# Optimization experiments

Measured on AMD Instinct MI355X. Metric: run time of the kernel, lower is better.

Reference implementation:

```python
import jax, jax.numpy as jnp
import numpy as np

B, L, DIM = 2, 2048, 1024
H, D = 16, 64  # n_heads, head_dim; H*D == DIM


def setup_inputs() -> dict:
    key = jax.random.key(0)
    ks = jax.random.split(key, 5)
    s = 0.02
    return {
        "x": jax.random.normal(ks[0], (B, L, DIM), dtype=jnp.float32),
        "Wq": jax.random.normal(ks[1], (DIM, H * D), dtype=jnp.float32) * s,
        "Wk": jax.random.normal(ks[2], (DIM, H * D), dtype=jnp.float32) * s,
        "Wv": jax.random.normal(ks[3], (DIM, H * D), dtype=jnp.float32) * s,
        "Wo": jax.random.normal(ks[4], (H * D, DIM), dtype=jnp.float32) * s,
    }


def reference(x, Wq, Wk, Wv, Wo):
    b, l, _ = x.shape
    scale = 1.0 / np.sqrt(D).astype(np.float32)
    # QKV projections -> [b, h, l, d]
    q = (x @ Wq).reshape(b, l, H, D).transpose(0, 2, 1, 3)
    k = (x @ Wk).reshape(b, l, H, D).transpose(0, 2, 1, 3)
    v = (x @ Wv).reshape(b, l, H, D).transpose(0, 2, 1, 3)
    # dense scores [b, h, l, l]
    scores = jnp.einsum("bhqd,bhkd->bhqk", q, k)
    # diagonal mask: each token cannot attend to itself
    diag = jnp.eye(l, dtype=bool)  # [l, l]
    scores = jnp.where(diag, -jnp.inf, scores)
    attn = jax.nn.softmax(scores * scale, axis=-1)
    out = jnp.einsum("bhqk,bhkd->bhqd", attn, v)
    out = out.transpose(0, 2, 1, 3).reshape(b, l, H * D)
    return out @ Wo
```

## Files before the change

### kernel.cpp

```cpp
#include <hip/hip_runtime.h>
#include <hip/hip_bf16.h>
#include <math.h>

#define L_SEQ 2048
#define DIMN  1024
#define NH    16
#define HD    64
#define NB    2
#define NTOK  (NB * L_SEQ)

typedef __attribute__((ext_vector_type(8))) short bf16x8;
typedef __attribute__((ext_vector_type(4))) float f32x4;
typedef __attribute__((ext_vector_type(16))) float f32x16;
typedef __attribute__((ext_vector_type(4))) short short4v;
typedef __attribute__((ext_vector_type(2))) unsigned uint32x2;

__device__ __forceinline__ short f2bf(float x) {
  return (short)__bfloat16_as_ushort(__float2bfloat16(x));
}

__device__ __forceinline__ unsigned cvt_pk_bf16(float lo, float hi) {
  unsigned r;
  asm("v_cvt_pk_bf16_f32 %0, %1, %2" : "=v"(r) : "v"(lo), "v"(hi));
  return r;
}

__device__ __forceinline__ void permlane32_swap(unsigned& a, unsigned& b) {
  asm volatile("v_permlane32_swap_b32 %0, %1" : "+v"(a), "+v"(b));
}

__device__ __forceinline__ void gload_lds16(const short* gsrc, char* lds_dst) {
  __builtin_amdgcn_global_load_lds(
      (const __attribute__((address_space(1))) void*)gsrc,
      (__attribute__((address_space(3))) void*)lds_dst, 16, 0, 0);
}

__global__ __launch_bounds__(256) void cast_x_k(const float* __restrict__ in,
                                                short* __restrict__ out) {
  const int i = (blockIdx.x * 256 + threadIdx.x) * 8;
  float4 a = *(const float4*)(in + i);
  float4 b = *(const float4*)(in + i + 4);
  bf16x8 o;
  o[0] = f2bf(a.x); o[1] = f2bf(a.y); o[2] = f2bf(a.z); o[3] = f2bf(a.w);
  o[4] = f2bf(b.x); o[5] = f2bf(b.y); o[6] = f2bf(b.z); o[7] = f2bf(b.w);
  *(bf16x8*)(out + i) = o;
}

__global__ __launch_bounds__(256) void castT_k(const float* __restrict__ W,
                                               short* __restrict__ Wt) {
  __shared__ float s[64][65];
  const int tid = threadIdx.x;
  const int k0 = blockIdx.y * 64, n0 = blockIdx.x * 64;
#pragma unroll
  for (int i = 0; i < 4; ++i) {
    int idx = i * 256 + tid;
    int r = idx >> 4, c = (idx & 15) * 4;
    float4 v = *(const float4*)(W + (size_t)(k0 + r) * DIMN + n0 + c);
    s[r][c] = v.x; s[r][c + 1] = v.y; s[r][c + 2] = v.z; s[r][c + 3] = v.w;
  }
  __syncthreads();
#pragma unroll
  for (int i = 0; i < 4; ++i) {
    int idx = i * 256 + tid;
    int r = idx >> 4, c = (idx & 15) * 4;
    short4v o = { f2bf(s[c][r]), f2bf(s[c + 1][r]), f2bf(s[c + 2][r]), f2bf(s[c + 3][r]) };
    *(short4v*)(Wt + (size_t)(n0 + r) * DIMN + k0 + c) = o;
  }
}

__global__ __launch_bounds__(256) void vT_k(const short* __restrict__ V,
                                            short* __restrict__ Vt) {
  __shared__ short s[64][72];
  const int tid = threadIdx.x;
  const int bh = blockIdx.y;
  const int l0 = blockIdx.x * 64;
  const int row = tid >> 2, c0 = (tid & 3) * 16;
  const short* Vh = V + (size_t)bh * L_SEQ * HD;
  bf16x8 a = *(const bf16x8*)(Vh + (size_t)(l0 + row) * HD + c0);
  bf16x8 b = *(const bf16x8*)(Vh + (size_t)(l0 + row) * HD + c0 + 8);
#pragma unroll
  for (int j = 0; j < 8; ++j) { s[c0 + j][row] = a[j]; s[c0 + 8 + j][row] = b[j]; }
  __syncthreads();
  short* Vth = Vt + (size_t)bh * HD * L_SEQ;
  bf16x8 o0 = *(const bf16x8*)&s[row][c0];
  bf16x8 o1 = *(const bf16x8*)&s[row][c0 + 8];
  *(bf16x8*)(Vth + (size_t)row * L_SEQ + l0 + c0) = o0;
  *(bf16x8*)(Vth + (size_t)row * L_SEQ + l0 + c0 + 8) = o1;
}

template <int MODE>
__global__ __launch_bounds__(256) void mm_k(const short* __restrict__ A,
                                            const short* __restrict__ B0,
                                            const short* __restrict__ B1,
                                            const short* __restrict__ B2,
                                            void* __restrict__ C0,
                                            void* __restrict__ C1,
                                            void* __restrict__ C2,
                                            float scale0) {
  __shared__ char smem[65536];
  const int tid  = threadIdx.x;
  const int lane = tid & 63, wv = tid >> 6;
  const int g = lane >> 4, r16 = lane & 15;
  const int wr = wv >> 1, wc = wv & 1;
  const int row0 = blockIdx.y * 128, col0 = blockIdx.x * 128;
  const int z = blockIdx.z;
  const short* Bt = (z == 0) ? B0 : (z == 1 ? B1 : B2);
  const float scale = (MODE == 0 && z == 0) ? scale0 : 1.0f;

  f32x4 acc[4][4];
#pragma unroll
  for (int mi = 0; mi < 4; ++mi)
#pragma unroll
    for (int ni = 0; ni < 4; ++ni) acc[mi][ni] = (f32x4){0.f, 0.f, 0.f, 0.f};

  auto stage = [&](int buf, int kt) {
    const int k0 = kt * 64;
    char* As = smem + buf * 32768;
    char* Bs = As + 16384;
#pragma unroll
    for (int j = 0; j < 4; ++j) {
      const int o = j * 4096 + wv * 1024 + lane * 16;
      const int row = o >> 7;
      const int slot = (o >> 4) & 7;
      const int ksrc = k0 + ((slot ^ (row & 7)) << 3);
      gload_lds16(A  + (size_t)(row0 + row) * DIMN + ksrc, As + j * 4096 + wv * 1024);
      gload_lds16(Bt + (size_t)(col0 + row) * DIMN + ksrc, Bs + j * 4096 + wv * 1024);
    }
  };

  auto compute = [&](int buf) {
    const char* As = smem + buf * 32768;
    const char* Bs = As + 16384;
#pragma unroll
    for (int ks = 0; ks < 2; ++ks) {
      bf16x8 a[4], b[4];
#pragma unroll
      for (int mi = 0; mi < 4; ++mi) {
        const int row = wr * 64 + mi * 16 + r16;
        const int slot = (ks * 4 + g) ^ (row & 7);
        a[mi] = *(const bf16x8*)(As + row * 128 + slot * 16);
      }
#pragma unroll
      for (int ni = 0; ni < 4; ++ni) {
        const int row = wc * 64 + ni * 16 + r16;
        const int slot = (ks * 4 + g) ^ (row & 7);
        b[ni] = *(const bf16x8*)(Bs + row * 128 + slot * 16);
      }
#pragma unroll
      for (int mi = 0; mi < 4; ++mi)
#pragma unroll
        for (int ni = 0; ni < 4; ++ni)
          acc[mi][ni] = __builtin_amdgcn_mfma_f32_16x16x32_bf16(a[mi], b[ni], acc[mi][ni], 0, 0, 0);
    }
  };

  stage(0, 0);
  __syncthreads();
  int cur = 0;
  for (int kt = 0; kt < DIMN / 64 - 1; ++kt) {
    stage(cur ^ 1, kt + 1);
    compute(cur);
    __syncthreads();
    cur ^= 1;
  }
  compute(cur);

  void* Cp = (z == 0) ? C0 : (z == 1 ? C1 : C2);
#pragma unroll
  for (int mi = 0; mi < 4; ++mi) {
#pragma unroll
    for (int reg = 0; reg < 4; ++reg) {
      const int t = row0 + wr * 64 + mi * 16 + 4 * g + reg;
#pragma unroll
      for (int ni = 0; ni < 4; ++ni) {
        const int n = col0 + wc * 64 + ni * 16 + r16;
        if (MODE == 0) {
          const int b = t >> 11, l = t & (L_SEQ - 1);
          const int h = n >> 6, d = n & 63;
          ((short*)Cp)[(((size_t)(b * NH + h)) * L_SEQ + l) * HD + d] =
              f2bf(acc[mi][ni][reg] * scale);
        } else {
          ((float*)Cp)[(size_t)t * DIMN + n] = acc[mi][ni][reg];
        }
      }
    }
  }
}

__global__ __launch_bounds__(256) void attn_k(const short* __restrict__ Q,
                                              const short* __restrict__ K,
                                              const short* __restrict__ Vt,
                                              short* __restrict__ O) {
  __shared__ char kv[2][16384];

  const int tid  = threadIdx.x;
  const int wave = tid >> 6, lane = tid & 63;
  const int h = lane >> 5, r32 = lane & 31;
  const int bh = blockIdx.y, qtile = blockIdx.x;
  const int qbase = qtile * 128 + wave * 32;
  const int dtile = qtile * 2 + (wave >> 1);
  const int qg = qbase + r32;

  const short* Qh  = Q  + (size_t)bh * L_SEQ * HD;
  const short* Kh  = K  + (size_t)bh * L_SEQ * HD;
  const short* Vth = Vt + (size_t)bh * HD * L_SEQ;

  bf16x8 qv[4];
#pragma unroll
  for (int ks = 0; ks < 4; ++ks)
    qv[ks] = *(const bf16x8*)(Qh + (size_t)qg * HD + ks * 16 + 8 * h);

  float lsum = 0.f;
  f32x16 o32[2];
#pragma unroll
  for (int db = 0; db < 2; ++db)
#pragma unroll
    for (int r = 0; r < 16; ++r) o32[db][r] = 0.f;

  const int sw = r32 & 7;
  const int rbase = r32 * 128;

  const int si1 = 256 + tid;
  const int row0s = tid >> 3,  c0s = (((tid & 7) ^ (row0s & 7)) << 3);
  const int row1s = si1 >> 3,  c1s = (((si1 & 7) ^ (row1s & 7)) << 3);
  const short* kp0 = Kh + (size_t)row0s * HD + c0s;
  const short* kp1 = Kh + (size_t)row1s * HD + c1s;
  const short* vp0 = Vth + (size_t)row0s * L_SEQ + c0s;
  const short* vp1 = Vth + (size_t)row1s * L_SEQ + c1s;
  const int ldo0 = tid * 16, ldo1 = si1 * 16;

  auto stage = [&](int buf) {
    char* base = kv[buf];
    gload_lds16(kp0, base + ldo0);
    gload_lds16(kp1, base + ldo1);
    gload_lds16(vp0, base + 8192 + ldo0);
    gload_lds16(vp1, base + 8192 + ldo1);
    kp0 += 64 * HD;
    kp1 += 64 * HD;
    vp0 += 64;
    vp1 += 64;
  };

  auto compute = [&](int buf, int kt) {
    const char* Kb = kv[buf];
    const char* Vb = kv[buf] + 8192;

    f32x16 sa[2];
#pragma unroll
    for (int kb = 0; kb < 2; ++kb)
#pragma unroll
      for (int r = 0; r < 16; ++r) sa[kb][r] = 0.f;
    __builtin_amdgcn_s_setprio(1);
#pragma unroll
    for (int kb = 0; kb < 2; ++kb)
#pragma unroll
      for (int ks = 0; ks < 4; ++ks) {
        bf16x8 ak = *(const bf16x8*)(Kb + (kb * 32) * 128 + rbase + ((2 * ks + h) ^ sw) * 16);
        sa[kb] = __builtin_amdgcn_mfma_f32_32x32x16_bf16(ak, qv[ks], sa[kb], 0, 0, 0);
      }
    __builtin_amdgcn_s_setprio(0);

    if (kt == dtile) {
      const int tgt = qg - kt * 64;
#pragma unroll
      for (int kb = 0; kb < 2; ++kb)
#pragma unroll
        for (int r = 0; r < 16; ++r)
          if (kb * 32 + (r & 3) + 8 * (r >> 2) + 4 * h == tgt) sa[kb][r] = -INFINITY;
    }

#pragma unroll
    for (int kb = 0; kb < 2; ++kb)
#pragma unroll
      for (int r = 0; r < 16; ++r) sa[kb][r] = exp2f(sa[kb][r]);
    float ps = 0.f;
#pragma unroll
    for (int kb = 0; kb < 2; ++kb) {
      float u0 = (sa[kb][0] + sa[kb][1]) + (sa[kb][2] + sa[kb][3]);
      float u1 = (sa[kb][4] + sa[kb][5]) + (sa[kb][6] + sa[kb][7]);
      float u2 = (sa[kb][8] + sa[kb][9]) + (sa[kb][10] + sa[kb][11]);
      float u3 = (sa[kb][12] + sa[kb][13]) + (sa[kb][14] + sa[kb][15]);
      ps += (u0 + u1) + (u2 + u3);
    }
    lsum += ps;

    bf16x8 bp[4];
#pragma unroll
    for (int kk = 0; kk < 4; ++kk) {
      const int kb = kk >> 1, s8 = (kk & 1) * 8;
      unsigned lo0 = cvt_pk_bf16(sa[kb][s8 + 0], sa[kb][s8 + 1]);
      unsigned lo1 = cvt_pk_bf16(sa[kb][s8 + 2], sa[kb][s8 + 3]);
      unsigned hi0 = cvt_pk_bf16(sa[kb][s8 + 4], sa[kb][s8 + 5]);
      unsigned hi1 = cvt_pk_bf16(sa[kb][s8 + 6], sa[kb][s8 + 7]);
      permlane32_swap(lo0, hi0);
      permlane32_swap(lo1, hi1);
      union { unsigned w[4]; bf16x8 v; } u;
      u.w[0] = lo0; u.w[1] = lo1; u.w[2] = hi0; u.w[3] = hi1;
      bp[kk] = u.v;
    }

    __builtin_amdgcn_s_setprio(1);
#pragma unroll
    for (int kk = 0; kk < 4; ++kk)
#pragma unroll
      for (int db = 0; db < 2; ++db) {
        bf16x8 av = *(const bf16x8*)(Vb + (db * 32) * 128 + rbase + ((2 * kk + h) ^ sw) * 16);
        o32[db] = __builtin_amdgcn_mfma_f32_32x32x16_bf16(av, bp[kk], o32[db], 0, 0, 0);
      }
    __builtin_amdgcn_s_setprio(0);
  };

  stage(0);
  __syncthreads();

  for (int t = 0; t < L_SEQ / 64; t += 2) {
    stage(1);
    compute(0, t);
    __syncthreads();
    if (t + 2 < L_SEQ / 64) stage(0);
    compute(1, t + 1);
    __syncthreads();
  }

  lsum += __shfl_xor(lsum, 32);

  const int b = bh >> 4, hh = bh & 15;
  const float inv = 1.0f / lsum;
  const size_t rowO = (size_t)(b * L_SEQ + qg) * DIMN + hh * HD;
#pragma unroll
  for (int db = 0; db < 2; ++db)
#pragma unroll
    for (int grp = 0; grp < 4; ++grp) {
      const int d0 = db * 32 + grp * 8 + 4 * h;
      uint32x2 ow = { cvt_pk_bf16(o32[db][grp * 4 + 0] * inv, o32[db][grp * 4 + 1] * inv),
                      cvt_pk_bf16(o32[db][grp * 4 + 2] * inv, o32[db][grp * 4 + 3] * inv) };
      *(uint32x2*)(O + rowO + d0) = ow;
    }
}

extern "C" void kernel_launch(void* const* d_in, const int* in_sizes, int n_in,
                              void* d_out, int out_size, void* d_ws, size_t ws_size,
                              hipStream_t stream) {
  const float* x  = (const float*)d_in[0];
  const float* Wq = (const float*)d_in[1];
  const float* Wk = (const float*)d_in[2];
  const float* Wv = (const float*)d_in[3];
  const float* Wo = (const float*)d_in[4];
  float* out = (float*)d_out;

  short* xb  = (short*)d_ws;
  short* Wqt = xb  + (size_t)NTOK * DIMN;
  short* Wkt = Wqt + (size_t)DIMN * DIMN;
  short* Wvt = Wkt + (size_t)DIMN * DIMN;
  short* Wot = Wvt + (size_t)DIMN * DIMN;
  short* Qb  = Wot + (size_t)DIMN * DIMN;
  short* Kb  = Qb  + (size_t)NTOK * DIMN;
  short* Vb  = Kb  + (size_t)NTOK * DIMN;
  short* Vtb = Vb  + (size_t)NTOK * DIMN;
  short* AO  = Vtb + (size_t)NTOK * DIMN;

  cast_x_k<<<NTOK * DIMN / (256 * 8), 256, 0, stream>>>(x, xb);
  const dim3 tgrid(DIMN / 64, DIMN / 64);
  castT_k<<<tgrid, 256, 0, stream>>>(Wq, Wqt);
  castT_k<<<tgrid, 256, 0, stream>>>(Wk, Wkt);
  castT_k<<<tgrid, 256, 0, stream>>>(Wv, Wvt);
  castT_k<<<tgrid, 256, 0, stream>>>(Wo, Wot);

  mm_k<0><<<dim3(DIMN / 128, NTOK / 128, 3), 256, 0, stream>>>(
      xb, Wqt, Wkt, Wvt, Qb, Kb, Vb, 0.125f * 1.4426950408889634f);

  vT_k<<<dim3(L_SEQ / 64, NB * NH), 256, 0, stream>>>(Vb, Vtb);

  attn_k<<<dim3(L_SEQ / 128, NB * NH), 256, 0, stream>>>(Qb, Kb, Vtb, AO);

  mm_k<1><<<dim3(DIMN / 128, NTOK / 128, 1), 256, 0, stream>>>(
      AO, Wot, Wot, Wot, out, out, out, 1.0f);
}
```

Measured before the change: 140.2 us.

## Triple-buffer K/V staging with vmcnt waits and remap block-to-head order

Switches the attention kernel's K/V LDS staging from double to triple buffering. Each step now waits only on the older outstanding global-to-LDS loads (vmcnt(4)) plus a single barrier, replacing the two full __syncthreads per pair of tiles, so loads run two tiles ahead of compute. It also remaps block IDs so consecutive blocks cover different batch-heads, which changes L2 locality and load spread. The extra buffer raises LDS use to 48KB per block, which may lower occupancy, and the hand-written waitcnt logic relies on exact counts of outstanding loads.

```diff
diff --git a/kernel.cpp b/kernel.cpp
--- a/kernel.cpp
+++ b/kernel.cpp
@@ -191,12 +191,16 @@
                                               const short* __restrict__ K,
                                               const short* __restrict__ Vt,
                                               short* __restrict__ O) {
-  __shared__ char kv[2][16384];
+  __shared__ char kv[3][16384];
 
   const int tid  = threadIdx.x;
   const int wave = tid >> 6, lane = tid & 63;
   const int h = lane >> 5, r32 = lane & 31;
-  const int bh = blockIdx.y, qtile = blockIdx.x;
+
+  const int id = blockIdx.x + 16 * blockIdx.y;
+  const int bh = (id & 7) * 4 + (id >> 7);
+  const int qtile = (id >> 3) & 15;
+
   const int qbase = qtile * 128 + wave * 32;
   const int dtile = qtile * 2 + (wave >> 1);
   const int qg = qbase + r32;
@@ -229,8 +233,7 @@
   const short* vp1 = Vth + (size_t)row1s * L_SEQ + c1s;
   const int ldo0 = tid * 16, ldo1 = si1 * 16;
 
-  auto stage = [&](int buf) {
-    char* base = kv[buf];
+  auto stage = [&](char* base) {
     gload_lds16(kp0, base + ldo0);
     gload_lds16(kp1, base + ldo1);
     gload_lds16(vp0, base + 8192 + ldo0);
@@ -241,9 +244,8 @@
     vp1 += 64;
   };
 
-  auto compute = [&](int buf, int kt) {
-    const char* Kb = kv[buf];
-    const char* Vb = kv[buf] + 8192;
+  auto compute = [&](const char* Kb, int kt) {
+    const char* Vb = Kb + 8192;
 
     f32x16 sa[2];
 #pragma unroll
@@ -310,17 +312,25 @@
     __builtin_amdgcn_s_setprio(0);
   };
 
-  stage(0);
-  __syncthreads();
-
-  for (int t = 0; t < L_SEQ / 64; t += 2) {
-    stage(1);
-    compute(0, t);
-    __syncthreads();
-    if (t + 2 < L_SEQ / 64) stage(0);
-    compute(1, t + 1);
-    __syncthreads();
-  }
+  auto step = [&](const char* cbuf, char* sbuf, int t, bool dostage, bool last) {
+    if (last) asm volatile("s_waitcnt vmcnt(0)" ::: "memory");
+    else      asm volatile("s_waitcnt vmcnt(4)" ::: "memory");
+    __builtin_amdgcn_s_barrier();
+    __builtin_amdgcn_sched_barrier(0);
+    if (dostage) stage(sbuf);
+    compute(cbuf, t);
+  };
+
+  stage(kv[0]);
+  stage(kv[1]);
+
+  for (int t = 0; t < 30; t += 3) {
+    step(kv[0], kv[2], t,     true, false);
+    step(kv[1], kv[0], t + 1, true, false);
+    step(kv[2], kv[1], t + 2, true, false);
+  }
+  step(kv[0], nullptr, 30, false, false);
+  step(kv[1], nullptr, 31, false, true);
 
   lsum += __shfl_xor(lsum, 32);
 
```

After: 138.6 us. No clear change (-1.1%).

## Split attention KV range in two blocks and combine partials in separate kernel

Applied to the files above, without the earlier changes.

Splits each query tile's key range across two blocks, doubling the attention grid to 1024 blocks. Each block writes unnormalized bf16 partial outputs and row sums, and a new combine kernel adds and normalizes them into the head-interleaved layout. The change also remaps block IDs so heads spread across XCDs, swaps the loop sync to an explicit vmcnt wait plus barrier, and uses the raw exp2 builtin. It adds an extra kernel launch and partial-output traffic, and summing partials is valid only because no running max is used, so there is no per-split rescale.

```diff
diff --git a/kernel.cpp b/kernel.cpp
--- a/kernel.cpp
+++ b/kernel.cpp
@@ -17,6 +17,11 @@
 
 __device__ __forceinline__ short f2bf(float x) {
   return (short)__bfloat16_as_ushort(__float2bfloat16(x));
+}
+__device__ __forceinline__ float bf2f(short x) {
+  union { unsigned u; float f; } c;
+  c.u = ((unsigned)(unsigned short)x) << 16;
+  return c.f;
 }
 
 __device__ __forceinline__ unsigned cvt_pk_bf16(float lo, float hi) {
@@ -190,16 +195,25 @@
 __global__ __launch_bounds__(256) void attn_k(const short* __restrict__ Q,
                                               const short* __restrict__ K,
                                               const short* __restrict__ Vt,
-                                              short* __restrict__ O) {
+                                              short* __restrict__ Op0,
+                                              short* __restrict__ Op1,
+                                              float* __restrict__ Lp) {
   __shared__ char kv[2][16384];
 
   const int tid  = threadIdx.x;
   const int wave = tid >> 6, lane = tid & 63;
   const int h = lane >> 5, r32 = lane & 31;
-  const int bh = blockIdx.y, qtile = blockIdx.x;
+
+  const int id = blockIdx.x + 32 * blockIdx.y;
+  const int j8 = id >> 3;
+  const int bh = (id & 7) * 4 + (j8 >> 5);
+  const int qtile = (j8 >> 1) & 15;
+  const int split = j8 & 1;
+
   const int qbase = qtile * 128 + wave * 32;
   const int dtile = qtile * 2 + (wave >> 1);
   const int qg = qbase + r32;
+  const int kbase = split * 16;
 
   const short* Qh  = Q  + (size_t)bh * L_SEQ * HD;
   const short* Kh  = K  + (size_t)bh * L_SEQ * HD;
@@ -223,14 +237,13 @@
   const int si1 = 256 + tid;
   const int row0s = tid >> 3,  c0s = (((tid & 7) ^ (row0s & 7)) << 3);
   const int row1s = si1 >> 3,  c1s = (((si1 & 7) ^ (row1s & 7)) << 3);
-  const short* kp0 = Kh + (size_t)row0s * HD + c0s;
-  const short* kp1 = Kh + (size_t)row1s * HD + c1s;
-  const short* vp0 = Vth + (size_t)row0s * L_SEQ + c0s;
-  const short* vp1 = Vth + (size_t)row1s * L_SEQ + c1s;
+  const short* kp0 = Kh + (size_t)(split * 1024 + row0s) * HD + c0s;
+  const short* kp1 = Kh + (size_t)(split * 1024 + row1s) * HD + c1s;
+  const short* vp0 = Vth + (size_t)row0s * L_SEQ + split * 1024 + c0s;
+  const short* vp1 = Vth + (size_t)row1s * L_SEQ + split * 1024 + c1s;
   const int ldo0 = tid * 16, ldo1 = si1 * 16;
 
-  auto stage = [&](int buf) {
-    char* base = kv[buf];
+  auto stage = [&](char* base) {
     gload_lds16(kp0, base + ldo0);
     gload_lds16(kp1, base + ldo1);
     gload_lds16(vp0, base + 8192 + ldo0);
@@ -241,9 +254,8 @@
     vp1 += 64;
   };
 
-  auto compute = [&](int buf, int kt) {
-    const char* Kb = kv[buf];
-    const char* Vb = kv[buf] + 8192;
+  auto compute = [&](const char* Kb, int kt) {
+    const char* Vb = Kb + 8192;
 
     f32x16 sa[2];
 #pragma unroll
@@ -272,7 +284,7 @@
 #pragma unroll
     for (int kb = 0; kb < 2; ++kb)
 #pragma unroll
-      for (int r = 0; r < 16; ++r) sa[kb][r] = exp2f(sa[kb][r]);
+      for (int r = 0; r < 16; ++r) sa[kb][r] = __builtin_amdgcn_exp2f(sa[kb][r]);
     float ps = 0.f;
 #pragma unroll
     for (int kb = 0; kb < 2; ++kb) {
@@ -310,32 +322,61 @@
     __builtin_amdgcn_s_setprio(0);
   };
 
-  stage(0);
-  __syncthreads();
-
-  for (int t = 0; t < L_SEQ / 64; t += 2) {
-    stage(1);
-    compute(0, t);
-    __syncthreads();
-    if (t + 2 < L_SEQ / 64) stage(0);
-    compute(1, t + 1);
-    __syncthreads();
+#define STEP(CBUF, SBUF, KT, DO_STAGE)                        \
+  do {                                                        \
+    asm volatile("s_waitcnt vmcnt(0)" ::: "memory");          \
+    __builtin_amdgcn_s_barrier();                             \
+    __builtin_amdgcn_sched_barrier(0);                        \
+    if (DO_STAGE) stage(SBUF);                                \
+    compute(CBUF, KT);                                        \
+  } while (0)
+
+  stage(kv[0]);
+  for (int i = 0; i < 14; i += 2) {
+    STEP(kv[0], kv[1], kbase + i,     true);
+    STEP(kv[1], kv[0], kbase + i + 1, true);
   }
+  STEP(kv[0], kv[1], kbase + 14, true);
+  STEP(kv[1], kv[0], kbase + 15, false);
+#undef STEP
 
   lsum += __shfl_xor(lsum, 32);
 
-  const int b = bh >> 4, hh = bh & 15;
-  const float inv = 1.0f / lsum;
-  const size_t rowO = (size_t)(b * L_SEQ + qg) * DIMN + hh * HD;
+  short* Opart = split ? Op1 : Op0;
+  const size_t rowO = ((size_t)bh * L_SEQ + qg) * HD;
 #pragma unroll
   for (int db = 0; db < 2; ++db)
 #pragma unroll
     for (int grp = 0; grp < 4; ++grp) {
       const int d0 = db * 32 + grp * 8 + 4 * h;
-      uint32x2 ow = { cvt_pk_bf16(o32[db][grp * 4 + 0] * inv, o32[db][grp * 4 + 1] * inv),
-                      cvt_pk_bf16(o32[db][grp * 4 + 2] * inv, o32[db][grp * 4 + 3] * inv) };
-      *(uint32x2*)(O + rowO + d0) = ow;
-    }
+      uint32x2 ow = { cvt_pk_bf16(o32[db][grp * 4 + 0], o32[db][grp * 4 + 1]),
+                      cvt_pk_bf16(o32[db][grp * 4 + 2], o32[db][grp * 4 + 3]) };
+      *(uint32x2*)(Opart + rowO + d0) = ow;
+    }
+  if (h == 0)
+    Lp[(size_t)(split * NB * NH + bh) * L_SEQ + qg] = lsum;
+}
+
+__global__ __launch_bounds__(256) void combine_k(const short* __restrict__ Op0,
+                                                 const short* __restrict__ Op1,
+                                                 const float* __restrict__ Lp,
+                                                 short* __restrict__ AO) {
+  const int idx = blockIdx.x * 256 + threadIdx.x;
+  const int d8 = (idx & 7) * 8;
+  const int q  = (idx >> 3) & (L_SEQ - 1);
+  const int bh = idx >> 14;
+  const size_t po = ((size_t)bh * L_SEQ + q) * HD + d8;
+  bf16x8 p0 = *(const bf16x8*)(Op0 + po);
+  bf16x8 p1 = *(const bf16x8*)(Op1 + po);
+  const float l0 = Lp[(size_t)bh * L_SEQ + q];
+  const float l1 = Lp[(size_t)(NB * NH + bh) * L_SEQ + q];
+  const float inv = 1.0f / (l0 + l1);
+  const int b = bh >> 4, hh = bh & 15;
+  bf16x8 o;
+#pragma unroll
+  for (int j = 0; j < 8; ++j)
+    o[j] = f2bf((bf2f(p0[j]) + bf2f(p1[j])) * inv);
+  *(bf16x8*)(AO + ((size_t)(b * L_SEQ + q)) * DIMN + hh * HD + d8) = o;
 }
 
 extern "C" void kernel_launch(void* const* d_in, const int* in_sizes, int n_in,
@@ -358,6 +399,9 @@
   short* Vb  = Kb  + (size_t)NTOK * DIMN;
   short* Vtb = Vb  + (size_t)NTOK * DIMN;
   short* AO  = Vtb + (size_t)NTOK * DIMN;
+  float* Lp  = (float*)(AO + (size_t)NTOK * DIMN);
+  short* Op0 = xb;
+  short* Op1 = Vb;
 
   cast_x_k<<<NTOK * DIMN / (256 * 8), 256, 0, stream>>>(x, xb);
   const dim3 tgrid(DIMN / 64, DIMN / 64);
@@ -371,7 +415,9 @@
 
   vT_k<<<dim3(L_SEQ / 64, NB * NH), 256, 0, stream>>>(Vb, Vtb);
 
-  attn_k<<<dim3(L_SEQ / 128, NB * NH), 256, 0, stream>>>(Qb, Kb, Vtb, AO);
+  attn_k<<<dim3(32, NB * NH), 256, 0, stream>>>(Qb, Kb, Vtb, Op0, Op1, Lp);
+
+  combine_k<<<2048, 256, 0, stream>>>(Op0, Op1, Lp, AO);
 
   mm_k<1><<<dim3(DIMN / 128, NTOK / 128, 1), 256, 0, stream>>>(
       AO, Wot, Wot, Wot, out, out, out, 1.0f);
```

New measurement: 131.8 us. -6.0%, faster.
